# Optimization experiments

Measured on AMD Instinct MI355X. Metric: run time of the kernel, lower is better.

The kernel has to match this reference:

```python
import jax, jax.numpy as jnp
import numpy as np

# DeformConv3d hyperparams (from init_kwargs)
STRIDE = (1, 1, 1)
PAD = (1, 1, 1)
DIL = (1, 1, 1)
GROUPS = 1
DEFORM_GROUPS = 1  # reference assumes dg == 1


def setup_inputs() -> dict:
    key = jax.random.key(0)
    k1, k2, k3, k4 = jax.random.split(key, 4)
    x = jax.random.normal(k1, (2, 32, 24, 24, 24), jnp.float32)
    # offset channels = 3 * dg * kD*kH*kW = 81, layout [k_idx, (dz,dy,dx)]
    offset = jax.random.normal(k2, (2, 81, 24, 24, 24), jnp.float32)
    weight = jax.random.normal(k3, (64, 32, 3, 3, 3), jnp.float32) * 0.05
    bias = jax.random.normal(k4, (64,), jnp.float32) * 0.05
    return {"x": x, "offset": offset, "weight": weight, "bias": bias}


def _deform_conv3d(x, offset, weight, bias):
    B, C, D, H, W = x.shape
    Cout, Cg, kD, kH, kW = weight.shape
    sD, sH, sW = STRIDE
    pD, pH, pW = PAD
    dD, dH, dW = DIL
    Kn = kD * kH * kW
    Do = (D + 2 * pD - dD * (kD - 1) - 1) // sD + 1
    Ho = (H + 2 * pH - dH * (kH - 1) - 1) // sH + 1
    Wo = (W + 2 * pW - dW * (kW - 1) - 1) // sW + 1
    N = Do * Ho * Wo

    # offset: [B, Kn*3, Do,Ho,Wo] -> [B, Kn, 3, N]
    off = offset.reshape(B, Kn, 3, N)

    # kernel tap grid [Kn]
    kz, ky, kx = jnp.meshgrid(jnp.arange(kD), jnp.arange(kH), jnp.arange(kW), indexing='ij')
    kz, ky, kx = kz.reshape(Kn), ky.reshape(Kn), kx.reshape(Kn)
    # output grid [N]
    oz, oy, ox = jnp.meshgrid(jnp.arange(Do), jnp.arange(Ho), jnp.arange(Wo), indexing='ij')
    oz, oy, ox = oz.reshape(N), oy.reshape(N), ox.reshape(N)

    # sampling coords [B, Kn, N]
    z = (oz[None, None, :] * sD - pD) + kz[None, :, None] * dD + off[:, :, 0]
    y = (oy[None, None, :] * sH - pH) + ky[None, :, None] * dH + off[:, :, 1]
    xx = (ox[None, None, :] * sW - pW) + kx[None, :, None] * dW + off[:, :, 2]

    z0 = jnp.floor(z); fz = z - z0
    y0 = jnp.floor(y); fy = y - y0
    x0 = jnp.floor(xx); fx = xx - x0

    x_flat = x.reshape(B, C, D * H * W)
    acc = jnp.zeros((B, C, Kn * N), x.dtype)
    # 8 trilinear corners (fixed small loop)
    for dz in (0, 1):
        iz = z0 + dz
        wz = fz if dz else (1.0 - fz)
        for dy in (0, 1):
            iy = y0 + dy
            wy = fy if dy else (1.0 - fy)
            for dx in (0, 1):
                ix = x0 + dx
                wx = fx if dx else (1.0 - fx)
                valid = ((iz >= 0) & (iz < D) & (iy >= 0) & (iy < H)
                         & (ix >= 0) & (ix < W))
                w = (wz * wy * wx) * valid.astype(x.dtype)  # [B,Kn,N]
                izc = jnp.clip(iz, 0, D - 1).astype(jnp.int32)
                iyc = jnp.clip(iy, 0, H - 1).astype(jnp.int32)
                ixc = jnp.clip(ix, 0, W - 1).astype(jnp.int32)
                idx = (izc * H + iyc) * W + ixc  # [B,Kn,N]
                g = jnp.take_along_axis(x_flat, idx.reshape(B, 1, Kn * N), axis=2)
                acc = acc + g * w.reshape(B, 1, Kn * N)

    # im2col columns ordered (c, kz, ky, kx) to match weight layout
    cols = acc.reshape(B, C * Kn, N)
    Cpg = C // GROUPS
    Opg = Cout // GROUPS
    cols_g = cols.reshape(B, GROUPS, Cpg * Kn, N)
    w_g = weight.reshape(GROUPS, Opg, Cpg * Kn)
    out = jnp.einsum('gok,bgkn->bgon', w_g, cols_g).reshape(B, Cout, N)
    out = out + bias[None, :, None]
    return out.reshape(B, Cout, Do, Ho, Wo)


def reference(x, offset, weight, bias):
    return _deform_conv3d(x, offset, weight, bias)
```

## Files before the change

### kernel.cpp

```cpp
#include <hip/hip_runtime.h>
#include <hip/hip_bf16.h>


constexpr int B   = 2;
constexpr int C   = 32;
constexpr int D   = 24, H = 24, W = 24;
constexpr int CO  = 64;
constexpr int KN  = 27;
constexpr int DHW = D * H * W;
constexpr int N   = DHW;
constexpr int CK  = C * KN;

constexpr int NPOS     = 16;
constexpr int NTAP     = NPOS * KN;
constexpr int TPB_MAIN = 448;
constexpr int PADR     = CK + 8;
constexpr int NBLK     = (B * N) / NPOS;

using short8 = __attribute__((ext_vector_type(8))) short;
using f32x4  = __attribute__((ext_vector_type(4))) float;

__device__ __forceinline__ unsigned short f2bf(float f) {
    unsigned int u = __float_as_uint(f);
    unsigned int r = (u + 0x7FFFu + ((u >> 16) & 1u)) >> 16;
    return (unsigned short)r;
}

__global__ __launch_bounds__(256)
void prep_x(const float* __restrict__ x, unsigned short* __restrict__ xT) {
    const int v   = blockIdx.x * 256 + threadIdx.x;
    const int b   = v / DHW;
    const int vox = v - b * DHW;
    int words[16];
    #pragma unroll
    for (int i = 0; i < 16; ++i) {
        const float f0 = x[((size_t)(b * C + 2 * i))     * DHW + vox];
        const float f1 = x[((size_t)(b * C + 2 * i + 1)) * DHW + vox];
        words[i] = (int)f2bf(f0) | ((int)f2bf(f1) << 16);
    }
    int4* dst = reinterpret_cast<int4*>(xT + (size_t)v * 32);
    dst[0] = make_int4(words[0],  words[1],  words[2],  words[3]);
    dst[1] = make_int4(words[4],  words[5],  words[6],  words[7]);
    dst[2] = make_int4(words[8],  words[9],  words[10], words[11]);
    dst[3] = make_int4(words[12], words[13], words[14], words[15]);
}

__global__ __launch_bounds__(256)
void prep_w(const float* __restrict__ wgt, unsigned short* __restrict__ wp) {
    const int idx   = blockIdx.x * 256 + threadIdx.x;
    const int j     = idx & 7;
    const int lane  = (idx >> 3) & 63;
    const int t     = idx >> 9;
    const int otile = t / 27;
    const int kstep = t - otile * 27;
    const int o     = otile * 16 + (lane & 15);
    const int c     = 8 * (lane >> 4) + j;
    wp[idx] = f2bf(wgt[(size_t)o * CK + c * KN + kstep]);
}

__global__ __launch_bounds__(TPB_MAIN)
void deform_main(const float* __restrict__ off,
                 const unsigned short* __restrict__ xT,
                 const unsigned short* __restrict__ wp,
                 const float* __restrict__ bias,
                 float* __restrict__ out) {
    __shared__ unsigned short s_vb[NPOS * PADR];

    const int tid   = threadIdx.x;
    const int blk   = blockIdx.x;
    const int n0    = blk * NPOS;
    const int b     = n0 / N;
    const int nbase = n0 - b * N;

    if (tid < NTAP) {
        const int p = tid & 15;
        const int k = tid >> 4;
        const int n = nbase + p;
        const int oz = n / 576;
        const int rr = n - oz * 576;
        const int oy = rr / 24;
        const int ox = rr - oy * 24;
        const int kz = k / 9;
        const int kr = k - kz * 9;
        const int ky = kr / 3;
        const int kx = kr - ky * 3;

        const float offz = off[((size_t)(b * 81 + k * 3 + 0)) * N + n];
        const float offy = off[((size_t)(b * 81 + k * 3 + 1)) * N + n];
        const float offx = off[((size_t)(b * 81 + k * 3 + 2)) * N + n];

        const float z  = (float)(oz - 1 + kz) + offz;
        const float y  = (float)(oy - 1 + ky) + offy;
        const float xx = (float)(ox - 1 + kx) + offx;
        const float zf = floorf(z), yf = floorf(y), xf = floorf(xx);
        const float fz = z - zf, fy = y - yf, fx = xx - xf;
        const int z0 = (int)zf, y0 = (int)yf, x0 = (int)xf;

        float acc[32];
        #pragma unroll
        for (int c = 0; c < 32; ++c) acc[c] = 0.0f;

        #pragma unroll
        for (int cz = 0; cz < 2; ++cz) {
            const int   iz = z0 + cz;
            const float wz = cz ? fz : 1.0f - fz;
            const bool  vz = (iz >= 0) && (iz < D);
            const int   izc = min(max(iz, 0), D - 1);
            #pragma unroll
            for (int cy = 0; cy < 2; ++cy) {
                const int   iy = y0 + cy;
                const float wy = cy ? fy : 1.0f - fy;
                const bool  vy = (iy >= 0) && (iy < H);
                const int   iyc = min(max(iy, 0), H - 1);
                #pragma unroll
                for (int cx = 0; cx < 2; ++cx) {
                    const int   ix = x0 + cx;
                    const float wx = cx ? fx : 1.0f - fx;
                    const bool  vd = vz && vy && (ix >= 0) && (ix < W);
                    const int   ixc = min(max(ix, 0), W - 1);
                    const float wc = vd ? (wz * wy * wx) : 0.0f;
                    const int4* src = reinterpret_cast<const int4*>(
                        xT + ((size_t)(b * DHW) + (izc * H + iyc) * W + ixc) * 32);
                    #pragma unroll
                    for (int q = 0; q < 4; ++q) {
                        const int4 dv = src[q];
                        const int w0 = dv.x, w1 = dv.y, w2 = dv.z, w3 = dv.w;
                        acc[q*8+0] += wc * __uint_as_float(((unsigned)w0) << 16);
                        acc[q*8+1] += wc * __uint_as_float(((unsigned)w0) & 0xFFFF0000u);
                        acc[q*8+2] += wc * __uint_as_float(((unsigned)w1) << 16);
                        acc[q*8+3] += wc * __uint_as_float(((unsigned)w1) & 0xFFFF0000u);
                        acc[q*8+4] += wc * __uint_as_float(((unsigned)w2) << 16);
                        acc[q*8+5] += wc * __uint_as_float(((unsigned)w2) & 0xFFFF0000u);
                        acc[q*8+6] += wc * __uint_as_float(((unsigned)w3) << 16);
                        acc[q*8+7] += wc * __uint_as_float(((unsigned)w3) & 0xFFFF0000u);
                    }
                }
            }
        }

        int4* dst = reinterpret_cast<int4*>(&s_vb[p * PADR + k * 32]);
        #define PACK2(i) ((int)f2bf(acc[2*(i)]) | ((int)f2bf(acc[2*(i)+1]) << 16))
        dst[0] = make_int4(PACK2(0),  PACK2(1),  PACK2(2),  PACK2(3));
        dst[1] = make_int4(PACK2(4),  PACK2(5),  PACK2(6),  PACK2(7));
        dst[2] = make_int4(PACK2(8),  PACK2(9),  PACK2(10), PACK2(11));
        dst[3] = make_int4(PACK2(12), PACK2(13), PACK2(14), PACK2(15));
        #undef PACK2
    }
    __syncthreads();

    const int wv = tid >> 6;
    if (wv < 4) {
        const int lane = tid & 63;
        f32x4 acc4 = {0.f, 0.f, 0.f, 0.f};
        const short8* wrow = reinterpret_cast<const short8*>(wp) + (wv * 27) * 64 + lane;
        const int lrow = (lane & 15) * PADR;
        const int lcol = (lane >> 4) * 8;
        #pragma unroll
        for (int ks = 0; ks < 27; ++ks) {
            const short8 a = wrow[ks * 64];
            const short8 bf = *reinterpret_cast<const short8*>(&s_vb[lrow + ks * 32 + lcol]);
            acc4 = __builtin_amdgcn_mfma_f32_16x16x32_bf16(a, bf, acc4, 0, 0, 0);
        }
        const int p = lane & 15;
        const int n = nbase + p;
        const int obase = wv * 16 + (lane >> 4) * 4;
        #pragma unroll
        for (int r = 0; r < 4; ++r) {
            const int o = obase + r;
            out[((size_t)(b * CO + o)) * N + n] = acc4[r] + bias[o];
        }
    }
}

extern "C" void kernel_launch(void* const* d_in, const int* in_sizes, int n_in,
                              void* d_out, int out_size, void* d_ws, size_t ws_size,
                              hipStream_t stream) {
    const float* x    = (const float*)d_in[0];
    const float* off  = (const float*)d_in[1];
    const float* wgt  = (const float*)d_in[2];
    const float* bias = (const float*)d_in[3];
    float* out = (float*)d_out;

    unsigned short* xT = (unsigned short*)d_ws;
    unsigned short* wp = (unsigned short*)((char*)d_ws + 1769472);

    prep_x<<<(B * DHW) / 256, 256, 0, stream>>>(x, xT);
    prep_w<<<(CO * CK) / 256, 256, 0, stream>>>(wgt, wp);
    deform_main<<<NBLK, TPB_MAIN, 0, stream>>>(off, xT, wp, bias, out);
}
```

Measured before the change: 116.1 us.

## Switch to fp16 packed trilinear gather, fp16 MFMA, and fuse prep kernels

Converts the staged x and weights from bf16 to fp16. The trilinear interpolation now accumulates in packed half-precision vector FMAs instead of 32 scalar fp32 FMAs with bit-unpacking, and the GEMM uses the f16 MFMA. Corner indices and weights are computed up front and the corner loads are batched four at a time, which exposes memory-level parallelism. The two prep kernels are merged into one launch, and prep_x now gives each thread one quarter of a voxel's channels. Accumulating in fp16 lowers accuracy and narrows the value range compared with fp32 accumulation.

Result: faster. 109.9 us (-5.4%).

```diff
diff --git a/kernel.cpp b/kernel.cpp
--- a/kernel.cpp
+++ b/kernel.cpp
@@ -1,5 +1,5 @@
 #include <hip/hip_runtime.h>
-#include <hip/hip_bf16.h>
+#include <hip/hip_fp16.h>
 
 
 constexpr int B   = 2;
@@ -17,54 +17,56 @@
 constexpr int PADR     = CK + 8;
 constexpr int NBLK     = (B * N) / NPOS;
 
-using short8 = __attribute__((ext_vector_type(8))) short;
-using f32x4  = __attribute__((ext_vector_type(4))) float;
+constexpr int PREPX_BLKS = (B * DHW * 4) / 256;
+constexpr int PREPW_BLKS = (CO * CK) / 256;
 
-__device__ __forceinline__ unsigned short f2bf(float f) {
-    unsigned int u = __float_as_uint(f);
-    unsigned int r = (u + 0x7FFFu + ((u >> 16) & 1u)) >> 16;
-    return (unsigned short)r;
+using h8v   = __attribute__((ext_vector_type(8))) _Float16;
+using f32x4 = __attribute__((ext_vector_type(4))) float;
+
+__device__ __forceinline__ h8v splat8(float w) {
+    const _Float16 h = (_Float16)w;
+    h8v r;
+    #pragma unroll
+    for (int i = 0; i < 8; ++i) r[i] = h;
+    return r;
 }
 
 __global__ __launch_bounds__(256)
-void prep_x(const float* __restrict__ x, unsigned short* __restrict__ xT) {
-    const int v   = blockIdx.x * 256 + threadIdx.x;
-    const int b   = v / DHW;
-    const int vox = v - b * DHW;
-    int words[16];
-    #pragma unroll
-    for (int i = 0; i < 16; ++i) {
-        const float f0 = x[((size_t)(b * C + 2 * i))     * DHW + vox];
-        const float f1 = x[((size_t)(b * C + 2 * i + 1)) * DHW + vox];
-        words[i] = (int)f2bf(f0) | ((int)f2bf(f1) << 16);
+void prep_fused(const float* __restrict__ x, const float* __restrict__ wgt,
+                _Float16* __restrict__ xT, _Float16* __restrict__ wp) {
+    const int bid = blockIdx.x;
+    if (bid < PREPX_BLKS) {
+        const int idx = bid * 256 + threadIdx.x;
+        const int v   = idx >> 2;
+        const int q   = idx & 3;
+        const int b   = v / DHW;
+        const int vox = v - b * DHW;
+        const float* src = x + ((size_t)(b * C + q * 8)) * DHW + vox;
+        _Float16 tmp[8];
+        #pragma unroll
+        for (int i = 0; i < 8; ++i) tmp[i] = (_Float16)src[(size_t)i * DHW];
+        *reinterpret_cast<int4*>(xT + (size_t)v * 32 + q * 8) =
+            *reinterpret_cast<const int4*>(tmp);
+    } else {
+        const int idx   = (bid - PREPX_BLKS) * 256 + threadIdx.x;
+        const int j     = idx & 7;
+        const int lane  = (idx >> 3) & 63;
+        const int t     = idx >> 9;
+        const int otile = t / 27;
+        const int kstep = t - otile * 27;
+        const int o     = otile * 16 + (lane & 15);
+        const int c     = 8 * (lane >> 4) + j;
+        wp[idx] = (_Float16)wgt[(size_t)o * CK + c * KN + kstep];
     }
-    int4* dst = reinterpret_cast<int4*>(xT + (size_t)v * 32);
-    dst[0] = make_int4(words[0],  words[1],  words[2],  words[3]);
-    dst[1] = make_int4(words[4],  words[5],  words[6],  words[7]);
-    dst[2] = make_int4(words[8],  words[9],  words[10], words[11]);
-    dst[3] = make_int4(words[12], words[13], words[14], words[15]);
-}
-
-__global__ __launch_bounds__(256)
-void prep_w(const float* __restrict__ wgt, unsigned short* __restrict__ wp) {
-    const int idx   = blockIdx.x * 256 + threadIdx.x;
-    const int j     = idx & 7;
-    const int lane  = (idx >> 3) & 63;
-    const int t     = idx >> 9;
-    const int otile = t / 27;
-    const int kstep = t - otile * 27;
-    const int o     = otile * 16 + (lane & 15);
-    const int c     = 8 * (lane >> 4) + j;
-    wp[idx] = f2bf(wgt[(size_t)o * CK + c * KN + kstep]);
 }
 
 __global__ __launch_bounds__(TPB_MAIN)
 void deform_main(const float* __restrict__ off,
-                 const unsigned short* __restrict__ xT,
-                 const unsigned short* __restrict__ wp,
+                 const _Float16* __restrict__ xT,
+                 const _Float16* __restrict__ wp,
                  const float* __restrict__ bias,
                  float* __restrict__ out) {
-    __shared__ unsigned short s_vb[NPOS * PADR];
+    __shared__ _Float16 s_vb[NPOS * PADR];
 
     const int tid   = threadIdx.x;
     const int blk   = blockIdx.x;
@@ -96,55 +98,50 @@
         const float fz = z - zf, fy = y - yf, fx = xx - xf;
         const int z0 = (int)zf, y0 = (int)yf, x0 = (int)xf;
 
-        float acc[32];
+        int   cidx[8];
+        float cw[8];
         #pragma unroll
-        for (int c = 0; c < 32; ++c) acc[c] = 0.0f;
+        for (int cr = 0; cr < 8; ++cr) {
+            const int cz = cr >> 2, cy = (cr >> 1) & 1, cx = cr & 1;
+            const int iz = z0 + cz, iy = y0 + cy, ix = x0 + cx;
+            const bool vd = ((unsigned)iz < (unsigned)D) &&
+                            ((unsigned)iy < (unsigned)H) &&
+                            ((unsigned)ix < (unsigned)W);
+            const int izc = min(max(iz, 0), D - 1);
+            const int iyc = min(max(iy, 0), H - 1);
+            const int ixc = min(max(ix, 0), W - 1);
+            cidx[cr] = (izc * H + iyc) * W + ixc;
+            const float wz = cz ? fz : 1.0f - fz;
+            const float wy = cy ? fy : 1.0f - fy;
+            const float wx = cx ? fx : 1.0f - fx;
+            cw[cr] = vd ? (wz * wy * wx) : 0.0f;
+        }
+
+        h8v acc0 = splat8(0.0f), acc1 = splat8(0.0f),
+            acc2 = splat8(0.0f), acc3 = splat8(0.0f);
+        const h8v* base = reinterpret_cast<const h8v*>(xT) + (size_t)b * DHW * 4;
 
         #pragma unroll
-        for (int cz = 0; cz < 2; ++cz) {
-            const int   iz = z0 + cz;
-            const float wz = cz ? fz : 1.0f - fz;
-            const bool  vz = (iz >= 0) && (iz < D);
-            const int   izc = min(max(iz, 0), D - 1);
+        for (int hb = 0; hb < 2; ++hb) {
+            h8v v[4][4];
             #pragma unroll
-            for (int cy = 0; cy < 2; ++cy) {
-                const int   iy = y0 + cy;
-                const float wy = cy ? fy : 1.0f - fy;
-                const bool  vy = (iy >= 0) && (iy < H);
-                const int   iyc = min(max(iy, 0), H - 1);
-                #pragma unroll
-                for (int cx = 0; cx < 2; ++cx) {
-                    const int   ix = x0 + cx;
-                    const float wx = cx ? fx : 1.0f - fx;
-                    const bool  vd = vz && vy && (ix >= 0) && (ix < W);
-                    const int   ixc = min(max(ix, 0), W - 1);
-                    const float wc = vd ? (wz * wy * wx) : 0.0f;
-                    const int4* src = reinterpret_cast<const int4*>(
-                        xT + ((size_t)(b * DHW) + (izc * H + iyc) * W + ixc) * 32);
-                    #pragma unroll
-                    for (int q = 0; q < 4; ++q) {
-                        const int4 dv = src[q];
-                        const int w0 = dv.x, w1 = dv.y, w2 = dv.z, w3 = dv.w;
-                        acc[q*8+0] += wc * __uint_as_float(((unsigned)w0) << 16);
-                        acc[q*8+1] += wc * __uint_as_float(((unsigned)w0) & 0xFFFF0000u);
-                        acc[q*8+2] += wc * __uint_as_float(((unsigned)w1) << 16);
-                        acc[q*8+3] += wc * __uint_as_float(((unsigned)w1) & 0xFFFF0000u);
-                        acc[q*8+4] += wc * __uint_as_float(((unsigned)w2) << 16);
-                        acc[q*8+5] += wc * __uint_as_float(((unsigned)w2) & 0xFFFF0000u);
-                        acc[q*8+6] += wc * __uint_as_float(((unsigned)w3) << 16);
-                        acc[q*8+7] += wc * __uint_as_float(((unsigned)w3) & 0xFFFF0000u);
-                    }
-                }
+            for (int cr = 0; cr < 4; ++cr) {
+                const h8v* s = base + (size_t)cidx[hb * 4 + cr] * 4;
+                v[cr][0] = s[0]; v[cr][1] = s[1];
+                v[cr][2] = s[2]; v[cr][3] = s[3];
+            }
+            #pragma unroll
+            for (int cr = 0; cr < 4; ++cr) {
+                const h8v w8 = splat8(cw[hb * 4 + cr]);
+                acc0 += v[cr][0] * w8;
+                acc1 += v[cr][1] * w8;
+                acc2 += v[cr][2] * w8;
+                acc3 += v[cr][3] * w8;
             }
         }
 
-        int4* dst = reinterpret_cast<int4*>(&s_vb[p * PADR + k * 32]);
-        #define PACK2(i) ((int)f2bf(acc[2*(i)]) | ((int)f2bf(acc[2*(i)+1]) << 16))
-        dst[0] = make_int4(PACK2(0),  PACK2(1),  PACK2(2),  PACK2(3));
-        dst[1] = make_int4(PACK2(4),  PACK2(5),  PACK2(6),  PACK2(7));
-        dst[2] = make_int4(PACK2(8),  PACK2(9),  PACK2(10), PACK2(11));
-        dst[3] = make_int4(PACK2(12), PACK2(13), PACK2(14), PACK2(15));
-        #undef PACK2
+        h8v* dst = reinterpret_cast<h8v*>(&s_vb[p * PADR + k * 32]);
+        dst[0] = acc0; dst[1] = acc1; dst[2] = acc2; dst[3] = acc3;
     }
     __syncthreads();
 
@@ -152,14 +149,14 @@
     if (wv < 4) {
         const int lane = tid & 63;
         f32x4 acc4 = {0.f, 0.f, 0.f, 0.f};
-        const short8* wrow = reinterpret_cast<const short8*>(wp) + (wv * 27) * 64 + lane;
+        const h8v* wrow = reinterpret_cast<const h8v*>(wp) + (wv * 27) * 64 + lane;
         const int lrow = (lane & 15) * PADR;
         const int lcol = (lane >> 4) * 8;
         #pragma unroll
         for (int ks = 0; ks < 27; ++ks) {
-            const short8 a = wrow[ks * 64];
-            const short8 bf = *reinterpret_cast<const short8*>(&s_vb[lrow + ks * 32 + lcol]);
-            acc4 = __builtin_amdgcn_mfma_f32_16x16x32_bf16(a, bf, acc4, 0, 0, 0);
+            const h8v a  = wrow[ks * 64];
+            const h8v bf = *reinterpret_cast<const h8v*>(&s_vb[lrow + ks * 32 + lcol]);
+            acc4 = __builtin_amdgcn_mfma_f32_16x16x32_f16(a, bf, acc4, 0, 0, 0);
         }
         const int p = lane & 15;
         const int n = nbase + p;
@@ -181,10 +178,9 @@
     const float* bias = (const float*)d_in[3];
     float* out = (float*)d_out;
 
-    unsigned short* xT = (unsigned short*)d_ws;
-    unsigned short* wp = (unsigned short*)((char*)d_ws + 1769472);
+    _Float16* xT = (_Float16*)d_ws;
+    _Float16* wp = (_Float16*)((char*)d_ws + 1769472);
 
-    prep_x<<<(B * DHW) / 256, 256, 0, stream>>>(x, xT);
-    prep_w<<<(CO * CK) / 256, 256, 0, stream>>>(wgt, wp);
+    prep_fused<<<PREPX_BLKS + PREPW_BLKS, 256, 0, stream>>>(x, wgt, xT, wp);
     deform_main<<<NBLK, TPB_MAIN, 0, stream>>>(off, xT, wp, bias, out);
 }
```
